# Kernel optimization log

Hardware: AMD Instinct MI355X
Metric: run time of the kernel (lower is better)

## Reference

```python
import jax, jax.numpy as jnp
import numpy as np

V, B, C, D, H, W = 5, 2, 32, 48, 128, 160


def setup_inputs() -> dict:
    key = jax.random.key(0)
    k1, k2, k3, k4 = jax.random.split(key, 4)
    features = jax.random.normal(k1, (V, B, C, H, W), jnp.float32)
    # Intrinsics (shared) and per-view extrinsics (identity rotation + small translation)
    K = np.eye(4, dtype=np.float32)
    K[0, 0] = 200.0; K[1, 1] = 200.0; K[0, 2] = W / 2.0; K[1, 2] = H / 2.0
    projs = np.zeros((B, V, 2, 4, 4), np.float32)
    for v in range(V):
        E = np.eye(4, dtype=np.float32)
        E[0, 3] = 0.1 * v
        E[1, 3] = 0.05 * v
        projs[:, v, 0] = E
        projs[:, v, 1] = K
    proj_matrices = jnp.asarray(projs)
    # Per-pixel depth sweep in [2, 10] with slight pixelwise perturbation
    d = jnp.linspace(2.0, 10.0, D, dtype=jnp.float32)
    depth_samples = jnp.broadcast_to(d[None, :, None, None], (B, D, H, W)) * (
        1.0 + 0.01 * jax.random.uniform(k2, (B, 1, H, W), jnp.float32))
    view_weights = jax.random.uniform(k3, (B, V - 1, H, W), jnp.float32, 0.1, 1.0)
    w_reg = 0.1 * jax.random.normal(k4, (C,), jnp.float32)
    b_reg = jnp.zeros((1,), jnp.float32)
    return {"features": features, "proj_matrices": proj_matrices,
            "depth_samples": depth_samples, "view_weights": view_weights,
            "w_reg": w_reg, "b_reg": b_reg}


def _bilinear_sample(img, px, py):
    # img: (C, H, W); px, py: (D, H, W) pixel coords. Zeros padding, align_corners=True.
    Cc, Hh, Ww = img.shape
    x0 = jnp.floor(px); y0 = jnp.floor(py)
    wx1 = px - x0; wx0 = 1.0 - wx1
    wy1 = py - y0; wy0 = 1.0 - wy1

    def gather(ix, iy, wgt):
        valid = (ix >= 0) & (ix <= Ww - 1) & (iy >= 0) & (iy <= Hh - 1)
        ixc = jnp.clip(ix, 0, Ww - 1).astype(jnp.int32)
        iyc = jnp.clip(iy, 0, Hh - 1).astype(jnp.int32)
        v = img[:, iyc, ixc]  # (C, D, H, W)
        return v * (wgt * valid)[None]

    return (gather(x0, y0, wx0 * wy0) + gather(x0 + 1, y0, wx1 * wy0)
            + gather(x0, y0 + 1, wx0 * wy1) + gather(x0 + 1, y0 + 1, wx1 * wy1))


def homo_warping(src_fea, src_proj, ref_proj, depth):
    # src_fea: (B,C,H,W); projs: (B,4,4); depth: (B,D,H,W) -> warped (B,C,D,H,W)
    Bn, Cc, Hh, Ww = src_fea.shape
    Dn = depth.shape[1]
    proj = src_proj @ jnp.linalg.inv(ref_proj)
    rot = proj[:, :3, :3]
    tr = proj[:, :3, 3]
    yy, xx = jnp.meshgrid(jnp.arange(Hh, dtype=src_fea.dtype),
                          jnp.arange(Ww, dtype=src_fea.dtype), indexing='ij')
    xyz = jnp.stack([xx.ravel(), yy.ravel(), jnp.ones(Hh * Ww, src_fea.dtype)])  # (3, HW)
    rot_xyz = jnp.einsum('bij,jn->bin', rot, xyz)  # (B, 3, HW)
    pxyz = rot_xyz[:, :, None, :] * depth.reshape(Bn, 1, Dn, Hh * Ww) + tr[:, :, None, None]
    z = pxyz[:, 2]
    valid = z > 1e-3
    zs = jnp.where(valid, z, 1.0)
    px = jnp.where(valid, pxyz[:, 0] / zs, -1e4).reshape(Bn, Dn, Hh, Ww)
    py = jnp.where(valid, pxyz[:, 1] / zs, -1e4).reshape(Bn, Dn, Hh, Ww)
    return jax.vmap(_bilinear_sample)(src_fea, px, py)


def _combined_proj(p):
    # p: (B, 2, 4, 4); new[:, :3, :4] = K[:3,:3] @ E[:3,:4]
    new = p[:, 0]
    return new.at[:, :3, :4].set(jnp.einsum('bij,bjk->bik', p[:, 1, :3, :3], p[:, 0, :3, :4]))


def reference(features, proj_matrices, depth_samples, view_weights, w_reg, b_reg):
    ref_fea = features[0]  # (B, C, H, W)
    Bn, Cc, Hh, Ww = ref_fea.shape
    Dn = depth_samples.shape[1]
    ref_proj_new = _combined_proj(proj_matrices[:, 0])
    vol_sum = jnp.zeros((Bn, Cc, Dn, Hh, Ww), ref_fea.dtype)
    wsum = jnp.full((Bn, 1, 1, Hh, Ww), 1e-5, ref_fea.dtype)
    nsrc = features.shape[0] - 1
    for i in range(nsrc):  # small fixed view loop
        src_proj_new = _combined_proj(proj_matrices[:, i + 1])
        warped = homo_warping(features[i + 1], src_proj_new, ref_proj_new, depth_samples)
        warped = warped * ref_fea[:, :, None]  # similarity volume
        w = view_weights[:, i][:, None, None]  # (B, 1, 1, H, W)
        vol_sum = vol_sum + warped * w
        wsum = wsum + w
    volume_aggregated = vol_sum / wsum
    # cost_reg_net stand-in: 1x1x1 conv over channels -> (B, D, H, W)
    prob_volume_pre = jnp.einsum('bcdhw,c->bdhw', volume_aggregated, w_reg) + b_reg
    prob_volume = jax.nn.softmax(prob_volume_pre, axis=1)
    depth = jnp.sum(prob_volume * depth_samples, axis=1)
    return (depth, jax.lax.stop_gradient(view_weights), prob_volume, volume_aggregated)
```

## Files before the change

### kernel.cpp

```cpp
#include <hip/hip_runtime.h>
#include <hip/hip_bf16.h>
#include <math.h>

#define V_ 5
#define B_ 2
#define C_ 32
#define D_ 48
#define H_ 128
#define W_ 160
#define NSRC 4
#define HW_ (H_ * W_)
#define DHW_ ((size_t)D_ * H_ * W_)
#define BHW_ (B_ * H_ * W_)
#define TOTAL_BDHW (B_ * D_ * H_ * W_)

#define NB_VOL (B_ * (H_ / 4) * (W_ / 16) * D_)
#define NB_VOL8 (NB_VOL / 8)

__device__ __forceinline__ void combined_proj(const float* p, double* P) {
    double E[16], K[16];
    for (int i = 0; i < 16; ++i) { E[i] = (double)p[i]; K[i] = (double)p[16 + i]; }
    for (int i = 0; i < 16; ++i) P[i] = E[i];
    for (int r = 0; r < 3; ++r)
        for (int c = 0; c < 4; ++c) {
            double s = 0.0;
            for (int j = 0; j < 3; ++j) s += K[r * 4 + j] * E[j * 4 + c];
            P[r * 4 + c] = s;
        }
}

__device__ void invert4(const double* A, double* out) {
    double M[4][8];
    for (int r = 0; r < 4; ++r)
        for (int c = 0; c < 4; ++c) {
            M[r][c] = A[r * 4 + c];
            M[r][c + 4] = (r == c) ? 1.0 : 0.0;
        }
    for (int col = 0; col < 4; ++col) {
        int piv = col;
        double best = fabs(M[col][col]);
        for (int r = col + 1; r < 4; ++r) {
            double v = fabs(M[r][col]);
            if (v > best) { best = v; piv = r; }
        }
        if (piv != col)
            for (int c = 0; c < 8; ++c) {
                double t = M[col][c]; M[col][c] = M[piv][c]; M[piv][c] = t;
            }
        double s = 1.0 / M[col][col];
        for (int c = 0; c < 8; ++c) M[col][c] *= s;
        for (int r = 0; r < 4; ++r)
            if (r != col) {
                double f = M[r][col];
                if (f != 0.0)
                    for (int c = 0; c < 8; ++c) M[r][c] -= f * M[col][c];
            }
    }
    for (int r = 0; r < 4; ++r)
        for (int c = 0; c < 4; ++c) out[r * 4 + c] = M[r][c + 4];
}

__global__ void proj_kernel(const float* __restrict__ pm, float* __restrict__ out) {
    int t = threadIdx.x;
    if (t >= B_ * NSRC) return;
    int b = t / NSRC, i = t % NSRC;
    double Pref[16], Psrc[16];
    combined_proj(pm + (size_t)((b * V_ + 0) * 2) * 16, Pref);
    combined_proj(pm + (size_t)((b * V_ + (i + 1)) * 2) * 16, Psrc);
    double inv[16];
    invert4(Pref, inv);
    double M[16];
    for (int r = 0; r < 4; ++r)
        for (int c = 0; c < 4; ++c) {
            double s = 0.0;
            for (int j = 0; j < 4; ++j) s += Psrc[r * 4 + j] * inv[j * 4 + c];
            M[r * 4 + c] = s;
        }
    float* o = out + t * 12;
    o[0] = (float)M[0];  o[1] = (float)M[1];  o[2] = (float)M[2];
    o[3] = (float)M[4];  o[4] = (float)M[5];  o[5] = (float)M[6];
    o[6] = (float)M[8];  o[7] = (float)M[9];  o[8] = (float)M[10];
    o[9] = (float)M[3];  o[10] = (float)M[7]; o[11] = (float)M[11];
}

__global__ __launch_bounds__(256) void transpose_bf16_kernel(
    const float* __restrict__ in, __hip_bfloat16* __restrict__ outT) {
    __shared__ float tile[32][33];
    int ibh = blockIdx.x;
    int w0 = blockIdx.y * 32;
    int h = ibh % H_;
    int ib = ibh / H_;
    int i = ib / B_, b = ib % B_;
    int tx = threadIdx.x, ty = threadIdx.y;
    const float* src = in + ((size_t)((i + 1) * B_ + b) * C_) * HW_ + (size_t)h * W_ + w0;
#pragma unroll
    for (int cs = 0; cs < 32; cs += 8)
        tile[cs + ty][tx] = src[(size_t)(cs + ty) * HW_ + tx];
    __syncthreads();
    __hip_bfloat16* dst = outT + ((size_t)ib * HW_ + (size_t)h * W_ + w0) * C_;
#pragma unroll
    for (int wv = 0; wv < 32; wv += 8)
        dst[(size_t)(wv + ty) * C_ + tx] = __float2bfloat16(tile[tx][wv + ty]);
}

__global__ __launch_bounds__(256) void vol_bf16_kernel(
    const __hip_bfloat16* __restrict__ featT, const float* __restrict__ features,
    const float* __restrict__ depth_samples, const float* __restrict__ view_weights,
    const float* __restrict__ w_reg, const float* __restrict__ b_reg,
    const float* __restrict__ projs, float* __restrict__ out_vol,
    float* __restrict__ out_pv) {
    int bid = blockIdx.x;
    int lid = (bid & 7) * NB_VOL8 + (bid >> 3);
    int d = lid % D_;
    int r = lid / D_;
    int wg = r % (W_ / 16);
    r /= (W_ / 16);
    int h4 = r % (H_ / 4);
    int b = r / (H_ / 4);

    int tix = threadIdx.x;
    int w16 = tix & 15;
    int c4 = (tix >> 4) & 3;
    int hg = tix >> 6;
    int h = h4 * 4 + hg;
    int w = wg * 16 + w16;
    int c0 = c4 * 8;

    int pix_idx = ((b * D_ + d) * H_ + h) * W_ + w;
    float xf = (float)w, yf = (float)h;
    float dep = depth_samples[pix_idx];

    float s[8];
#pragma unroll
    for (int k = 0; k < 8; ++k) s[k] = 0.f;
    float wsum = 1e-5f;

#pragma unroll
    for (int i = 0; i < NSRC; ++i) {
        float vw = view_weights[((size_t)(b * NSRC + i) * H_ + h) * W_ + w];
        wsum += vw;
        const float* pr = projs + (b * NSRC + i) * 12;
        float rx = pr[0] * xf + pr[1] * yf + pr[2];
        float ry = pr[3] * xf + pr[4] * yf + pr[5];
        float rz = pr[6] * xf + pr[7] * yf + pr[8];
        float pxn = rx * dep + pr[9];
        float pyn = ry * dep + pr[10];
        float z = rz * dep + pr[11];
        bool valid = z > 0.001f;
        float zs = valid ? z : 1.f;
        float px = valid ? pxn / zs : -10000.f;
        float py = valid ? pyn / zs : -10000.f;

        float x0f = floorf(px), y0f = floorf(py);
        float x1f = x0f + 1.f, y1f = y0f + 1.f;
        float wx1 = px - x0f, wx0 = 1.f - wx1;
        float wy1 = py - y0f, wy0 = 1.f - wy1;
        bool vx0 = (x0f >= 0.f) && (x0f <= (float)(W_ - 1));
        bool vx1 = (x1f >= 0.f) && (x1f <= (float)(W_ - 1));
        bool vy0 = (y0f >= 0.f) && (y0f <= (float)(H_ - 1));
        bool vy1 = (y1f >= 0.f) && (y1f <= (float)(H_ - 1));
        int ix0 = (int)fminf(fmaxf(x0f, 0.f), (float)(W_ - 1));
        int ix1 = (int)fminf(fmaxf(x1f, 0.f), (float)(W_ - 1));
        int iy0 = (int)fminf(fmaxf(y0f, 0.f), (float)(H_ - 1));
        int iy1 = (int)fminf(fmaxf(y1f, 0.f), (float)(H_ - 1));
        float w00 = wx0 * wy0 * ((vx0 && vy0) ? vw : 0.f);
        float w10 = wx1 * wy0 * ((vx1 && vy0) ? vw : 0.f);
        float w01 = wx0 * wy1 * ((vx0 && vy1) ? vw : 0.f);
        float w11 = wx1 * wy1 * ((vx1 && vy1) ? vw : 0.f);

        const __hip_bfloat16* base = featT + (size_t)(i * B_ + b) * HW_ * C_ + c0;
        uint4 u00 = *(const uint4*)(base + (size_t)(iy0 * W_ + ix0) * C_);
        uint4 u10 = *(const uint4*)(base + (size_t)(iy0 * W_ + ix1) * C_);
        uint4 u01 = *(const uint4*)(base + (size_t)(iy1 * W_ + ix0) * C_);
        uint4 u11 = *(const uint4*)(base + (size_t)(iy1 * W_ + ix1) * C_);

#define ACC1(u, wgt)                                                     \
        {                                                                \
            s[0] += __uint_as_float((u).x << 16) * (wgt);                \
            s[1] += __uint_as_float((u).x & 0xffff0000u) * (wgt);        \
            s[2] += __uint_as_float((u).y << 16) * (wgt);                \
            s[3] += __uint_as_float((u).y & 0xffff0000u) * (wgt);        \
            s[4] += __uint_as_float((u).z << 16) * (wgt);                \
            s[5] += __uint_as_float((u).z & 0xffff0000u) * (wgt);        \
            s[6] += __uint_as_float((u).w << 16) * (wgt);                \
            s[7] += __uint_as_float((u).w & 0xffff0000u) * (wgt);        \
        }
        ACC1(u00, w00)
        ACC1(u10, w10)
        ACC1(u01, w01)
        ACC1(u11, w11)
#undef ACC1
    }

    float inv_wsum = 1.f / wsum;
    size_t obase = (size_t)b * C_ * DHW_ + (size_t)d * HW_ + (size_t)h * W_ + w;
    const float* refp = features + ((size_t)b * C_ + c0) * HW_ + (size_t)h * W_ + w;
    float pv = 0.f;
#pragma unroll
    for (int k = 0; k < 8; ++k) {
        float vc = refp[(size_t)k * HW_] * s[k] * inv_wsum;
        __builtin_nontemporal_store(vc, &out_vol[obase + (size_t)(c0 + k) * DHW_]);
        pv += vc * w_reg[c0 + k];
    }
    pv += __shfl_xor(pv, 16, 64);
    pv += __shfl_xor(pv, 32, 64);
    if (c4 == 0) out_pv[pix_idx] = pv + b_reg[0];
}

__global__ __launch_bounds__(256) void vol_fallback_kernel(
    const float* __restrict__ feat, const float* __restrict__ depth_samples,
    const float* __restrict__ view_weights, const float* __restrict__ w_reg,
    const float* __restrict__ b_reg, const float* __restrict__ projs,
    float* __restrict__ out_vol, float* __restrict__ out_pv) {
    int tid = blockIdx.x * 256 + threadIdx.x;
    if (tid >= TOTAL_BDHW) return;
    int w = tid % W_;
    int t2 = tid / W_;
    int h = t2 % H_;
    t2 /= H_;
    int d = t2 % D_;
    int b = t2 / D_;

    float xf = (float)w, yf = (float)h;
    float dep = depth_samples[tid];
    float s[C_];
#pragma unroll
    for (int c = 0; c < C_; ++c) s[c] = 0.f;
    float wsum = 1e-5f;

    for (int i = 0; i < NSRC; ++i) {
        float vw = view_weights[((size_t)(b * NSRC + i) * H_ + h) * W_ + w];
        wsum += vw;
        const float* pr = projs + (b * NSRC + i) * 12;
        float rx = pr[0] * xf + pr[1] * yf + pr[2];
        float ry = pr[3] * xf + pr[4] * yf + pr[5];
        float rz = pr[6] * xf + pr[7] * yf + pr[8];
        float pxn = rx * dep + pr[9];
        float pyn = ry * dep + pr[10];
        float z = rz * dep + pr[11];
        bool valid = z > 0.001f;
        float zs = valid ? z : 1.f;
        float px = valid ? pxn / zs : -10000.f;
        float py = valid ? pyn / zs : -10000.f;
        float x0f = floorf(px), y0f = floorf(py);
        float x1f = x0f + 1.f, y1f = y0f + 1.f;
        float wx1 = px - x0f, wx0 = 1.f - wx1;
        float wy1 = py - y0f, wy0 = 1.f - wy1;
        bool vx0 = (x0f >= 0.f) && (x0f <= (float)(W_ - 1));
        bool vx1 = (x1f >= 0.f) && (x1f <= (float)(W_ - 1));
        bool vy0 = (y0f >= 0.f) && (y0f <= (float)(H_ - 1));
        bool vy1 = (y1f >= 0.f) && (y1f <= (float)(H_ - 1));
        int ix0 = (int)fminf(fmaxf(x0f, 0.f), (float)(W_ - 1));
        int ix1 = (int)fminf(fmaxf(x1f, 0.f), (float)(W_ - 1));
        int iy0 = (int)fminf(fmaxf(y0f, 0.f), (float)(H_ - 1));
        int iy1 = (int)fminf(fmaxf(y1f, 0.f), (float)(H_ - 1));
        float w00 = wx0 * wy0 * ((vx0 && vy0) ? vw : 0.f);
        float w10 = wx1 * wy0 * ((vx1 && vy0) ? vw : 0.f);
        float w01 = wx0 * wy1 * ((vx0 && vy1) ? vw : 0.f);
        float w11 = wx1 * wy1 * ((vx1 && vy1) ? vw : 0.f);
        const float* base = feat + (size_t)((i + 1) * B_ + b) * C_ * HW_;
        const float* q00 = base + (size_t)iy0 * W_ + ix0;
        const float* q10 = base + (size_t)iy0 * W_ + ix1;
        const float* q01 = base + (size_t)iy1 * W_ + ix0;
        const float* q11 = base + (size_t)iy1 * W_ + ix1;
#pragma unroll
        for (int c = 0; c < C_; ++c)
            s[c] += q00[(size_t)c * HW_] * w00 + q10[(size_t)c * HW_] * w10 +
                    q01[(size_t)c * HW_] * w01 + q11[(size_t)c * HW_] * w11;
    }
    float inv_wsum = 1.f / wsum;
    size_t obase = (size_t)b * C_ * DHW_ + (size_t)d * HW_ + (size_t)h * W_ + w;
    const float* refp = feat + (size_t)b * C_ * HW_ + (size_t)h * W_ + w;
    float pv = 0.f;
#pragma unroll
    for (int c = 0; c < C_; ++c) {
        float vc = refp[(size_t)c * HW_] * s[c] * inv_wsum;
        out_vol[obase + (size_t)c * DHW_] = vc;
        pv += vc * w_reg[c];
    }
    out_pv[tid] = pv + b_reg[0];
}

__global__ __launch_bounds__(256) void finalize_kernel(
    const float* __restrict__ ds, const float* __restrict__ vw,
    float* __restrict__ out_depth, float* __restrict__ out_vw,
    float* __restrict__ pv) {
    int tid = blockIdx.x * 256 + threadIdx.x;
    if (tid >= BHW_) return;
    int w = tid % W_;
    int t2 = tid / W_;
    int h = t2 % H_;
    int b = t2 / H_;
    size_t base = (size_t)b * DHW_ + (size_t)h * W_ + w;

    float p[D_];
    float m = -1e30f;
#pragma unroll
    for (int d = 0; d < D_; ++d) {
        p[d] = pv[base + (size_t)d * HW_];
        m = fmaxf(m, p[d]);
    }
    float ssum = 0.f;
#pragma unroll
    for (int d = 0; d < D_; ++d) {
        p[d] = expf(p[d] - m);
        ssum += p[d];
    }
    float inv = 1.f / ssum;
    float dep = 0.f;
#pragma unroll
    for (int d = 0; d < D_; ++d) {
        float pr = p[d] * inv;
        pv[base + (size_t)d * HW_] = pr;
        dep += pr * ds[base + (size_t)d * HW_];
    }
    out_depth[tid] = dep;
#pragma unroll
    for (int k = 0; k < NSRC; ++k)
        out_vw[tid + k * BHW_] = vw[tid + k * BHW_];
}

extern "C" void kernel_launch(void* const* d_in, const int* in_sizes, int n_in,
                              void* d_out, int out_size, void* d_ws, size_t ws_size,
                              hipStream_t stream) {
    const float* features = (const float*)d_in[0];
    const float* pm       = (const float*)d_in[1];
    const float* dsamp    = (const float*)d_in[2];
    const float* vweights = (const float*)d_in[3];
    const float* w_reg    = (const float*)d_in[4];
    const float* b_reg    = (const float*)d_in[5];

    float* out = (float*)d_out;
    float* out_depth = out;
    float* out_vw    = out + 40960;
    float* out_prob  = out + 204800;
    float* out_vol   = out + 2170880;

    float* wsf   = (float*)d_ws;
    float* projb = wsf;
    __hip_bfloat16* featT = (__hip_bfloat16*)(wsf + 128);

    size_t need = 512 + (size_t)NSRC * B_ * HW_ * C_ * sizeof(__hip_bfloat16);
    bool chlast = (ws_size >= need);

    hipLaunchKernelGGL(proj_kernel, dim3(1), dim3(64), 0, stream, pm, projb);

    if (chlast) {
        hipLaunchKernelGGL(transpose_bf16_kernel, dim3(NSRC * B_ * H_, W_ / 32),
                           dim3(32, 8), 0, stream, features, featT);
        hipLaunchKernelGGL(vol_bf16_kernel, dim3(NB_VOL), dim3(256), 0, stream,
                           featT, features, dsamp, vweights, w_reg, b_reg, projb,
                           out_vol, out_prob);
    } else {
        hipLaunchKernelGGL(vol_fallback_kernel, dim3((TOTAL_BDHW + 255) / 256),
                           dim3(256), 0, stream, features, dsamp, vweights, w_reg,
                           b_reg, projb, out_vol, out_prob);
    }

    hipLaunchKernelGGL(finalize_kernel, dim3(BHW_ / 256), dim3(256), 0, stream,
                       dsamp, vweights, out_depth, out_vw, out_prob);
}
```

Measured before the change: 163.2 us.

## Split projection math across threads and share bilinear weights via LDS

In the old kernel, each of the 4 channel-group threads per pixel recomputed all four view projections and bilinear weights. Now the 256 threads split that work, one (pixel, view) pair each, and write the weights, byte offsets and view weight to shared memory. After a barrier, every thread reads them back for its gather and accumulate. The divides are also replaced with hardware reciprocal approximations and w_reg is loaded as float4, which adds LDS traffic and a sync in exchange for removing redundant ALU work and may slightly change rounding.

```diff
diff --git a/kernel.cpp b/kernel.cpp
--- a/kernel.cpp
+++ b/kernel.cpp
@@ -103,12 +103,14 @@
         dst[(size_t)(wv + ty) * C_ + tx] = __float2bfloat16(tile[tx][wv + ty]);
 }
 
-__global__ __launch_bounds__(256) void vol_bf16_kernel(
+__global__ __launch_bounds__(256) void vol_split_kernel(
     const __hip_bfloat16* __restrict__ featT, const float* __restrict__ features,
     const float* __restrict__ depth_samples, const float* __restrict__ view_weights,
     const float* __restrict__ w_reg, const float* __restrict__ b_reg,
     const float* __restrict__ projs, float* __restrict__ out_vol,
     float* __restrict__ out_pv) {
+    __shared__ float lds[NSRC * 64 * 12];
+
     int bid = blockIdx.x;
     int lid = (bid & 7) * NB_VOL8 + (bid >> 3);
     int d = lid % D_;
@@ -119,27 +121,17 @@
     int b = r / (H_ / 4);
 
     int tix = threadIdx.x;
-    int w16 = tix & 15;
-    int c4 = (tix >> 4) & 3;
-    int hg = tix >> 6;
-    int h = h4 * 4 + hg;
-    int w = wg * 16 + w16;
-    int c0 = c4 * 8;
-
-    int pix_idx = ((b * D_ + d) * H_ + h) * W_ + w;
-    float xf = (float)w, yf = (float)h;
-    float dep = depth_samples[pix_idx];
-
-    float s[8];
-#pragma unroll
-    for (int k = 0; k < 8; ++k) s[k] = 0.f;
-    float wsum = 1e-5f;
-
-#pragma unroll
-    for (int i = 0; i < NSRC; ++i) {
-        float vw = view_weights[((size_t)(b * NSRC + i) * H_ + h) * W_ + w];
-        wsum += vw;
-        const float* pr = projs + (b * NSRC + i) * 12;
+
+    {
+        int p = tix & 63;
+        int v = tix >> 6;
+        int w = wg * 16 + (p & 15);
+        int h = h4 * 4 + (p >> 4);
+        int pix = ((b * D_ + d) * H_ + h) * W_ + w;
+        float dep = depth_samples[pix];
+        float vw = view_weights[((size_t)(b * NSRC + v) * H_ + h) * W_ + w];
+        const float* pr = projs + (b * NSRC + v) * 12;
+        float xf = (float)w, yf = (float)h;
         float rx = pr[0] * xf + pr[1] * yf + pr[2];
         float ry = pr[3] * xf + pr[4] * yf + pr[5];
         float rz = pr[6] * xf + pr[7] * yf + pr[8];
@@ -147,32 +139,64 @@
         float pyn = ry * dep + pr[10];
         float z = rz * dep + pr[11];
         bool valid = z > 0.001f;
-        float zs = valid ? z : 1.f;
-        float px = valid ? pxn / zs : -10000.f;
-        float py = valid ? pyn / zs : -10000.f;
+        float zr = __builtin_amdgcn_rcpf(valid ? z : 1.f);
+        float px = valid ? pxn * zr : -10000.f;
+        float py = valid ? pyn * zr : -10000.f;
 
         float x0f = floorf(px), y0f = floorf(py);
-        float x1f = x0f + 1.f, y1f = y0f + 1.f;
         float wx1 = px - x0f, wx0 = 1.f - wx1;
         float wy1 = py - y0f, wy0 = 1.f - wy1;
         bool vx0 = (x0f >= 0.f) && (x0f <= (float)(W_ - 1));
-        bool vx1 = (x1f >= 0.f) && (x1f <= (float)(W_ - 1));
+        bool vx1 = (x0f >= -1.f) && (x0f <= (float)(W_ - 2));
         bool vy0 = (y0f >= 0.f) && (y0f <= (float)(H_ - 1));
-        bool vy1 = (y1f >= 0.f) && (y1f <= (float)(H_ - 1));
+        bool vy1 = (y0f >= -1.f) && (y0f <= (float)(H_ - 2));
         int ix0 = (int)fminf(fmaxf(x0f, 0.f), (float)(W_ - 1));
-        int ix1 = (int)fminf(fmaxf(x1f, 0.f), (float)(W_ - 1));
+        int ix1 = (int)fminf(fmaxf(x0f + 1.f, 0.f), (float)(W_ - 1));
         int iy0 = (int)fminf(fmaxf(y0f, 0.f), (float)(H_ - 1));
-        int iy1 = (int)fminf(fmaxf(y1f, 0.f), (float)(H_ - 1));
+        int iy1 = (int)fminf(fmaxf(y0f + 1.f, 0.f), (float)(H_ - 1));
         float w00 = wx0 * wy0 * ((vx0 && vy0) ? vw : 0.f);
         float w10 = wx1 * wy0 * ((vx1 && vy0) ? vw : 0.f);
         float w01 = wx0 * wy1 * ((vx0 && vy1) ? vw : 0.f);
         float w11 = wx1 * wy1 * ((vx1 && vy1) ? vw : 0.f);
 
-        const __hip_bfloat16* base = featT + (size_t)(i * B_ + b) * HW_ * C_ + c0;
-        uint4 u00 = *(const uint4*)(base + (size_t)(iy0 * W_ + ix0) * C_);
-        uint4 u10 = *(const uint4*)(base + (size_t)(iy0 * W_ + ix1) * C_);
-        uint4 u01 = *(const uint4*)(base + (size_t)(iy1 * W_ + ix0) * C_);
-        uint4 u11 = *(const uint4*)(base + (size_t)(iy1 * W_ + ix1) * C_);
+        int o00 = (iy0 * W_ + ix0) << 6;
+        int o10 = (iy0 * W_ + ix1) << 6;
+        int o01 = (iy1 * W_ + ix0) << 6;
+        int o11 = (iy1 * W_ + ix1) << 6;
+
+        float* row = lds + (size_t)((v << 6) + p) * 12;
+        *(float4*)row = make_float4(w00, w10, w01, w11);
+        *(int4*)(row + 4) = make_int4(o00, o10, o01, o11);
+        row[8] = vw;
+    }
+    __syncthreads();
+
+    int w16 = tix & 15;
+    int c4 = (tix >> 4) & 3;
+    int hg = tix >> 6;
+    int p = w16 + 16 * hg;
+    int h = h4 * 4 + hg;
+    int w = wg * 16 + w16;
+    int c0 = c4 * 8;
+    int c16 = c4 * 16;
+
+    float s[8];
+#pragma unroll
+    for (int k = 0; k < 8; ++k) s[k] = 0.f;
+    float wsum = 1e-5f;
+
+#pragma unroll
+    for (int v = 0; v < NSRC; ++v) {
+        const float* row = lds + (size_t)((v << 6) + p) * 12;
+        float4 wv4 = *(const float4*)row;
+        int4 ov = *(const int4*)(row + 4);
+        wsum += row[8];
+
+        const char* fv = (const char*)(featT + (size_t)(v * B_ + b) * HW_ * C_);
+        uint4 u00 = *(const uint4*)(fv + (ov.x + c16));
+        uint4 u10 = *(const uint4*)(fv + (ov.y + c16));
+        uint4 u01 = *(const uint4*)(fv + (ov.z + c16));
+        uint4 u11 = *(const uint4*)(fv + (ov.w + c16));
 
 #define ACC1(u, wgt)                                                     \
         {                                                                \
@@ -185,22 +209,26 @@
             s[6] += __uint_as_float((u).w << 16) * (wgt);                \
             s[7] += __uint_as_float((u).w & 0xffff0000u) * (wgt);        \
         }
-        ACC1(u00, w00)
-        ACC1(u10, w10)
-        ACC1(u01, w01)
-        ACC1(u11, w11)
+        ACC1(u00, wv4.x)
+        ACC1(u10, wv4.y)
+        ACC1(u01, wv4.z)
+        ACC1(u11, wv4.w)
 #undef ACC1
     }
 
-    float inv_wsum = 1.f / wsum;
+    float inv_wsum = __builtin_amdgcn_rcpf(wsum);
+    int pix_idx = ((b * D_ + d) * H_ + h) * W_ + w;
     size_t obase = (size_t)b * C_ * DHW_ + (size_t)d * HW_ + (size_t)h * W_ + w;
     const float* refp = features + ((size_t)b * C_ + c0) * HW_ + (size_t)h * W_ + w;
+    float4 wr0 = *(const float4*)(w_reg + c0);
+    float4 wr1 = *(const float4*)(w_reg + c0 + 4);
+    float wrr[8] = {wr0.x, wr0.y, wr0.z, wr0.w, wr1.x, wr1.y, wr1.z, wr1.w};
     float pv = 0.f;
 #pragma unroll
     for (int k = 0; k < 8; ++k) {
         float vc = refp[(size_t)k * HW_] * s[k] * inv_wsum;
         __builtin_nontemporal_store(vc, &out_vol[obase + (size_t)(c0 + k) * DHW_]);
-        pv += vc * w_reg[c0 + k];
+        pv += vc * wrr[k];
     }
     pv += __shfl_xor(pv, 16, 64);
     pv += __shfl_xor(pv, 32, 64);
@@ -348,7 +376,7 @@
     if (chlast) {
         hipLaunchKernelGGL(transpose_bf16_kernel, dim3(NSRC * B_ * H_, W_ / 32),
                            dim3(32, 8), 0, stream, features, featT);
-        hipLaunchKernelGGL(vol_bf16_kernel, dim3(NB_VOL), dim3(256), 0, stream,
+        hipLaunchKernelGGL(vol_split_kernel, dim3(NB_VOL), dim3(256), 0, stream,
                            featT, features, dsamp, vweights, w_reg, b_reg, projb,
                            out_vol, out_prob);
     } else {
```

New measurement: 164.9 us. Within noise of the previous version (+1.0%).
